# Optimization experiments

Hardware: AMD Instinct MI355X
Metric: run time of the kernel (lower is better)

Reference implementation:

```python
import jax, jax.numpy as jnp
import numpy as np

WINDOW = 16  # signature_window_size
D = 6        # input_path_dim


def _mlp(x, Ws, bs, final_act):
    for W, b in zip(Ws[:-1], bs[:-1]):
        x = jax.nn.softplus(W @ x + b)
    return final_act(Ws[-1] @ x + bs[-1])


def _windowed_logsig(xs):
    """Depth-2 log-signature of each window of the (piecewise-linear) path.
    Returns level-1 increments [n, D] and Levy areas [n, D, D] (antisymmetric)."""
    dx = xs[1:] - xs[:-1]                              # [T-1, D]
    n = dx.shape[0] // WINDOW
    dxw = dx[: n * WINDOW].reshape(n, WINDOW, D)
    lvl1 = dxw.sum(axis=1)                             # [n, D]
    cum = jnp.cumsum(dxw, axis=1) - dxw                # exclusive prefix sums
    cross = jnp.einsum('nwi,nwj->nij', cum, dxw)
    area = 0.5 * (cross - jnp.swapaxes(cross, 1, 2))   # [n, D, D]
    return lvl1, area


def setup_inputs() -> dict:
    key = jax.random.key(0)
    ks = jax.random.split(key, 9)
    S, H, OUT = 128, 128, 10
    B, T = 8, 513

    def lin(k, o, i):
        return jax.random.normal(k, (o, i), jnp.float32) / np.sqrt(i)

    return {
        'x': jax.random.normal(ks[0], (B, T, D), jnp.float32),
        'W_i0': lin(ks[1], H, D), 'b_i0': jnp.zeros((H,), jnp.float32),
        'W_i1': lin(ks[2], H, H), 'b_i1': jnp.zeros((H,), jnp.float32),
        'W_i2': lin(ks[3], S, H), 'b_i2': jnp.zeros((S,), jnp.float32),
        'W_v0': lin(ks[4], H, S), 'b_v0': jnp.zeros((H,), jnp.float32),
        'W_v1': lin(ks[5], H, H), 'b_v1': jnp.zeros((H,), jnp.float32),
        'W_v2': lin(ks[6], D * S, H), 'b_v2': jnp.zeros((D * S,), jnp.float32),
        'W_r': lin(ks[7], OUT, S), 'b_r': jnp.zeros((OUT,), jnp.float32),
    }


def reference(x, W_i0, b_i0, W_i1, b_i1, W_i2, b_i2,
              W_v0, b_v0, W_v1, b_v1, W_v2, b_v2, W_r, b_r):
    S = W_i2.shape[0]
    init_mlp = lambda z: _mlp(z, (W_i0, W_i1, W_i2), (b_i0, b_i1, b_i2), lambda u: u)
    # Vector fields V_i: R^S -> R^S, one per input channel (split_multi_vector_field)
    vf = lambda h: _mlp(h, (W_v0, W_v1, W_v2), (b_v0, b_v1, b_v2), jnp.tanh).reshape(D, S)
    mask = jnp.triu(jnp.ones((D, D), x.dtype), 1)  # Lyndon words i<j at depth 2

    def single(xs):  # xs: [T, D]
        lvl1, area = _windowed_logsig(xs)
        h0 = init_mlp(xs[0])

        def step(h, sig):
            l1, a = sig
            V = vf(h)                                  # [D, S]
            J = jax.jacfwd(vf)(h)                      # [D, S, S], J[j,b,a]=dV_j[b]/dh[a]
            M = jnp.einsum('jba,ia->ijb', J, V)        # (DV_j)(h) V_i(h)
            brack = M - jnp.swapaxes(M, 0, 1)          # Lie brackets [V_i, V_j](h)
            h_new = h + jnp.einsum('i,ib->b', l1, V) \
                      + jnp.einsum('ij,ijb->b', a * mask, brack)  # log-ODE step
            return h_new, h_new

        _, hist = jax.lax.scan(step, h0, (lvl1, area))
        hist = jnp.concatenate([h0[None], hist], axis=0)   # [n+1, S]
        return hist @ W_r.T + b_r                          # evolving readout

    return jax.vmap(single)(x)
```

## Files before the change

kernel.cpp:

```cpp
#include <hip/hip_runtime.h>
#include <math.h>

#define D    6
#define S    128
#define H    128
#define WIN  16
#define BB   8
#define TT   513
#define NW   32
#define OUTD 10

__device__ float g_lvl1[BB * NW * D];
__device__ float g_area[BB * NW * D * D];
__device__ float g_h0[BB * S];
__device__ float g_hist[BB * (NW + 1) * S];
__device__ float4 g_W2p[3 * 16 * 512];

__device__ __forceinline__ float sp(float x) {
    return (x > 20.f) ? x : log1pf(expf(x));
}
__device__ __forceinline__ float sigm(float x) {
    return 1.f / (1.f + expf(-x));
}
__device__ __forceinline__ float dot4(float4 a, float4 b, float acc) {
    return fmaf(a.x, b.x, fmaf(a.y, b.y, fmaf(a.z, b.z, fmaf(a.w, b.w, acc))));
}

#define O_W0   0
#define O_W1   16384
#define O_PS   32768
#define O_U    35840
#define O_T    36608
#define O_V    37376
#define O_H    38144
#define O_U1   38400
#define O_U2   38528
#define O_SG1  38656
#define O_SG2  38784
#define O_B0   38912
#define O_B1   39040
#define O_SIG  39168
#define SMTOT  39256

__global__ __launch_bounds__(512) void k_pack(const float* __restrict__ Wv2) {
    const float4* W24 = (const float4*)Wv2;
    int e = blockIdx.x * 512 + threadIdx.x;
    if (e < 3 * 16 * 512) {
        int ptr = e >> 13;
        int rem = e & 8191;
        int i   = rem >> 9;
        int tid = rem & 511;
        int r0 = tid >> 1, kh = tid & 1;
        int row = r0 + ptr * 256;
        g_W2p[e] = W24[row * 32 + kh * 16 + i];
    }
}

__global__ __launch_bounds__(256) void k_sig(
        const float* __restrict__ x,
        const float* __restrict__ Wi0, const float* __restrict__ bi0,
        const float* __restrict__ Wi1, const float* __restrict__ bi1,
        const float* __restrict__ Wi2, const float* __restrict__ bi2) {
    const int b = blockIdx.x;
    const int tid = threadIdx.x;
    __shared__ float dxs[NW][WIN][D];
    __shared__ float cums[NW][WIN][D];
    __shared__ float ua[H], ub[H];

    const float* xb = x + (size_t)b * TT * D;

    if (tid < NW * D) {
        int w = tid / D, i = tid % D;
        float run = 0.f;
        float prev = xb[(w * WIN) * D + i];
        for (int k = 0; k < WIN; ++k) {
            float cur = xb[(w * WIN + k + 1) * D + i];
            float d = cur - prev; prev = cur;
            dxs[w][k][i] = d;
            cums[w][k][i] = run;
            run += d;
        }
        g_lvl1[(b * NW + w) * D + i] = run;
    }
    __syncthreads();
    for (int e = tid; e < NW * D * D; e += blockDim.x) {
        int w = e / (D * D); int rem = e % (D * D);
        int i = rem / D, j = rem % D;
        float s = 0.f;
        for (int k = 0; k < WIN; ++k)
            s += cums[w][k][i] * dxs[w][k][j] - cums[w][k][j] * dxs[w][k][i];
        g_area[(b * NW + w) * (D * D) + rem] = 0.5f * s;
    }
    if (tid < H) {
        float z = bi0[tid];
        for (int k = 0; k < D; ++k) z += Wi0[tid * D + k] * xb[k];
        ua[tid] = sp(z);
    }
    __syncthreads();
    if (tid < H) {
        float z = bi1[tid];
        for (int k = 0; k < H; ++k) z += Wi1[tid * H + k] * ua[k];
        ub[tid] = sp(z);
    }
    __syncthreads();
    if (tid < H) {
        float z = bi2[tid];
        for (int k = 0; k < H; ++k) z += Wi2[tid * H + k] * ub[k];
        g_h0[b * S + tid] = z;
    }
}

__global__ __launch_bounds__(512, 2) void k_scan(
        const float* __restrict__ bv0, const float* __restrict__ bv1,
        const float* __restrict__ bv2,
        const float* __restrict__ Wv0, const float* __restrict__ Wv1) {
    __shared__ float sm[SMTOT];
    const int tid = threadIdx.x;
    const int b = blockIdx.x;
    const int r   = tid & 127;
    const int c4  = tid >> 7;
    const int key = r & 7;
    const int kh = tid & 1;
    const int r0 = tid >> 1, r1 = r0 + 256, r2 = r0 + 512;
    const int jA = tid >> 8, jB = 2 + jA, jC = 4 + jA;

    {
        float4* d = (float4*)(sm + O_W0);
        const float4* s0 = (const float4*)Wv0;
        const float4* s1 = (const float4*)Wv1;
        for (int i = tid; i < 4096; i += 512) { d[i] = s0[i]; d[4096 + i] = s1[i]; }
    }
    const float4* WAp = g_W2p + tid;
    const float4* WBp = g_W2p + 8192 + tid;
    const float4* WCp = g_W2p + 16384 + tid;
    if (tid < 128) {
        sm[O_B0 + tid] = bv0[tid]; sm[O_B1 + tid] = bv1[tid];
        float h0v = g_h0[b * 128 + tid];
        sm[O_H + tid] = h0v;
        g_hist[(b * (NW + 1)) * 128 + tid] = h0v;
    }
    if (tid >= 448) {
        int q = tid - 448;
        if (q < 42)
            sm[O_SIG + q] = (q < 6) ? g_lvl1[(b * NW) * 6 + q]
                                    : g_area[(b * NW) * 36 + q - 6];
    }
    __syncthreads();

    const float4* W04 = (const float4*)(sm + O_W0);
    const float4* W14 = (const float4*)(sm + O_W1);

    int p = 0;
    for (int t = 0; t < NW; ++t) {
        float rsig = 0.f;
        if (tid >= 448) {
            int q = tid - 448;
            if (q < 42 && t + 1 < NW)
                rsig = (q < 6) ? g_lvl1[(b * NW + t + 1) * 6 + q]
                               : g_area[(b * NW + t + 1) * 36 + q - 6];
        }
        const int sb = O_SIG + (t & 1) * 44;

        {
            float a = 0.f;
            const float4* H4 = (const float4*)(sm + O_H + p * 128);
            #pragma unroll
            for (int q = 0; q < 8; ++q) {
                int qq = c4 * 8 + (q ^ key);
                a = dot4(W04[r * 32 + qq], H4[qq], a);
            }
            sm[O_PS + (c4 * 6) * 128 + r] = a;
        }
        __syncthreads();
        if (tid < 128) {
            float z = sm[O_B0 + tid];
            #pragma unroll
            for (int c = 0; c < 4; ++c) z += sm[O_PS + (c * 6) * 128 + tid];
            sm[O_U1 + tid] = sp(z); sm[O_SG1 + tid] = sigm(z);
        }
        __syncthreads();
        {
            float a = 0.f;
            const float4* U14 = (const float4*)(sm + O_U1);
            #pragma unroll
            for (int q = 0; q < 8; ++q) {
                int qq = c4 * 8 + (q ^ key);
                a = dot4(W14[r * 32 + qq], U14[qq], a);
            }
            sm[O_PS + (c4 * 6) * 128 + r] = a;
        }
        __syncthreads();
        if (tid < 128) {
            float z = sm[O_B1 + tid];
            #pragma unroll
            for (int c = 0; c < 4; ++c) z += sm[O_PS + (c * 6) * 128 + tid];
            sm[O_U2 + tid] = sp(z); sm[O_SG2 + tid] = sigm(z);
        }
        __syncthreads();
        {
            float acc0 = 0.f, acc1 = 0.f, acc2 = 0.f;
            const float4* U24 = (const float4*)(sm + O_U2) + kh * 16;
            #pragma unroll 4
            for (int i = 0; i < 16; ++i) {
                float4 u = U24[i];
                acc0 = dot4(WAp[i * 512], u, acc0);
                acc1 = dot4(WBp[i * 512], u, acc1);
                acc2 = dot4(WCp[i * 512], u, acc2);
            }
            sm[O_PS + kh * 768 + r0] = acc0;
            sm[O_PS + kh * 768 + r1] = acc1;
            sm[O_PS + kh * 768 + r2] = acc2;
        }
        __syncthreads();
        {
            sm[O_V + tid] = tanhf(bv2[tid] + sm[O_PS + tid] + sm[O_PS + 768 + tid]);
            if (tid < 256) {
                int e = tid + 512;
                sm[O_V + e] = tanhf(bv2[e] + sm[O_PS + e] + sm[O_PS + 768 + e]);
            }
        }
        __syncthreads();
        {
            #pragma unroll
            for (int s = 0; s < 2; ++s) {
                int e = tid + s * 512;
                if (s == 0 || tid < 256) {
                    int jj = e >> 7, rr = e & 127;
                    float u = 0.f;
                    #pragma unroll
                    for (int i = 0; i < 6; ++i)
                        u = fmaf(sm[sb + 6 + i * 6 + jj], sm[O_V + i * 128 + rr], u);
                    sm[O_U + jj * 128 + rr] = u;
                }
            }
            if (tid < 128) {
                float xh = sm[O_H + p * 128 + tid];
                #pragma unroll
                for (int i = 0; i < 6; ++i)
                    xh = fmaf(sm[sb + i], sm[O_V + i * 128 + tid], xh);
                sm[O_H + (p ^ 1) * 128 + tid] = xh;
            }
        }
        __syncthreads();
        {
            float a0 = 0.f, a1 = 0.f, a2 = 0.f, a3 = 0.f, a4 = 0.f, a5 = 0.f;
            const float4* U4 = (const float4*)(sm + O_U);
            #pragma unroll
            for (int q = 0; q < 8; ++q) {
                int qq = c4 * 8 + (q ^ key);
                float4 w = W04[r * 32 + qq];
                a0 = dot4(w, U4[qq], a0);
                a1 = dot4(w, U4[32 + qq], a1);
                a2 = dot4(w, U4[64 + qq], a2);
                a3 = dot4(w, U4[96 + qq], a3);
                a4 = dot4(w, U4[128 + qq], a4);
                a5 = dot4(w, U4[160 + qq], a5);
            }
            sm[O_PS + (c4 * 6 + 0) * 128 + r] = a0;
            sm[O_PS + (c4 * 6 + 1) * 128 + r] = a1;
            sm[O_PS + (c4 * 6 + 2) * 128 + r] = a2;
            sm[O_PS + (c4 * 6 + 3) * 128 + r] = a3;
            sm[O_PS + (c4 * 6 + 4) * 128 + r] = a4;
            sm[O_PS + (c4 * 6 + 5) * 128 + r] = a5;
        }
        __syncthreads();
        {
            #pragma unroll
            for (int s = 0; s < 2; ++s) {
                int e = tid + s * 512;
                if (s == 0 || tid < 256) {
                    int jj = e >> 7, rr = e & 127;
                    float sv = sm[O_PS + jj * 128 + rr] + sm[O_PS + (6 + jj) * 128 + rr]
                             + sm[O_PS + (12 + jj) * 128 + rr] + sm[O_PS + (18 + jj) * 128 + rr];
                    sm[O_T + jj * 128 + rr] = sm[O_SG1 + rr] * sv;
                }
            }
        }
        __syncthreads();
        {
            float a0 = 0.f, a1 = 0.f, a2 = 0.f, a3 = 0.f, a4 = 0.f, a5 = 0.f;
            const float4* T4 = (const float4*)(sm + O_T);
            #pragma unroll
            for (int q = 0; q < 8; ++q) {
                int qq = c4 * 8 + (q ^ key);
                float4 w = W14[r * 32 + qq];
                a0 = dot4(w, T4[qq], a0);
                a1 = dot4(w, T4[32 + qq], a1);
                a2 = dot4(w, T4[64 + qq], a2);
                a3 = dot4(w, T4[96 + qq], a3);
                a4 = dot4(w, T4[128 + qq], a4);
                a5 = dot4(w, T4[160 + qq], a5);
            }
            sm[O_PS + (c4 * 6 + 0) * 128 + r] = a0;
            sm[O_PS + (c4 * 6 + 1) * 128 + r] = a1;
            sm[O_PS + (c4 * 6 + 2) * 128 + r] = a2;
            sm[O_PS + (c4 * 6 + 3) * 128 + r] = a3;
            sm[O_PS + (c4 * 6 + 4) * 128 + r] = a4;
            sm[O_PS + (c4 * 6 + 5) * 128 + r] = a5;
        }
        __syncthreads();
        {
            #pragma unroll
            for (int s = 0; s < 2; ++s) {
                int e = tid + s * 512;
                if (s == 0 || tid < 256) {
                    int jj = e >> 7, rr = e & 127;
                    float sv = sm[O_PS + jj * 128 + rr] + sm[O_PS + (6 + jj) * 128 + rr]
                             + sm[O_PS + (12 + jj) * 128 + rr] + sm[O_PS + (18 + jj) * 128 + rr];
                    sm[O_U + jj * 128 + rr] = sm[O_SG2 + rr] * sv;
                }
            }
        }
        __syncthreads();
        {
            float acc0 = 0.f, acc1 = 0.f, acc2 = 0.f;
            const float4* TA = (const float4*)(sm + O_U) + jA * 32 + kh * 16;
            const float4* TB = (const float4*)(sm + O_U) + jB * 32 + kh * 16;
            const float4* TC = (const float4*)(sm + O_U) + jC * 32 + kh * 16;
            #pragma unroll 4
            for (int i = 0; i < 16; ++i) {
                acc0 = dot4(WAp[i * 512], TA[i], acc0);
                acc1 = dot4(WBp[i * 512], TB[i], acc1);
                acc2 = dot4(WCp[i * 512], TC[i], acc2);
            }
            sm[O_PS + kh * 768 + r0] = acc0;
            sm[O_PS + kh * 768 + r1] = acc1;
            sm[O_PS + kh * 768 + r2] = acc2;
        }
        __syncthreads();
        {
            float v = sm[O_V + tid];
            sm[O_T + tid] = (1.f - v * v) * (sm[O_PS + tid] + sm[O_PS + 768 + tid]);
            if (tid < 256) {
                int e = tid + 512;
                float v2 = sm[O_V + e];
                sm[O_T + e] = (1.f - v2 * v2) * (sm[O_PS + e] + sm[O_PS + 768 + e]);
            }
        }
        __syncthreads();
        if (tid < 128) {
            float xh = sm[O_H + (p ^ 1) * 128 + tid];
            #pragma unroll
            for (int j = 0; j < 6; ++j) xh += sm[O_T + j * 128 + tid];
            sm[O_H + (p ^ 1) * 128 + tid] = xh;
            g_hist[(b * (NW + 1) + t + 1) * 128 + tid] = xh;
        }
        if (tid >= 448) {
            int q = tid - 448;
            if (q < 42 && t + 1 < NW)
                sm[O_SIG + ((t + 1) & 1) * 44 + q] = rsig;
        }
        p ^= 1;
        __syncthreads();
    }
}

__global__ __launch_bounds__(384) void k_read(const float* __restrict__ Wr,
                                              const float* __restrict__ br,
                                              float* __restrict__ out) {
    const int b = blockIdx.x, e = threadIdx.x;
    if (e < (NW + 1) * OUTD) {
        int t = e / OUTD, o = e % OUTD;
        float z = br[o];
        const float4* hrow = (const float4*)&g_hist[(b * (NW + 1) + t) * 128];
        const float4* wrow = (const float4*)&Wr[o * 128];
        float z0 = 0, z1 = 0, z2 = 0, z3 = 0;
        #pragma unroll 8
        for (int s4 = 0; s4 < 32; ++s4) {
            float4 hv = hrow[s4]; float4 wv = wrow[s4];
            z0 = fmaf(hv.x, wv.x, z0); z1 = fmaf(hv.y, wv.y, z1);
            z2 = fmaf(hv.z, wv.z, z2); z3 = fmaf(hv.w, wv.w, z3);
        }
        out[(b * (NW + 1) + t) * OUTD + o] = z + ((z0 + z1) + (z2 + z3));
    }
}

extern "C" void kernel_launch(void* const* d_in, const int* in_sizes, int n_in,
                              void* d_out, int out_size, void* d_ws, size_t ws_size,
                              hipStream_t stream) {
    const float* x   = (const float*)d_in[0];
    const float* Wi0 = (const float*)d_in[1];
    const float* bi0 = (const float*)d_in[2];
    const float* Wi1 = (const float*)d_in[3];
    const float* bi1 = (const float*)d_in[4];
    const float* Wi2 = (const float*)d_in[5];
    const float* bi2 = (const float*)d_in[6];
    const float* Wv0 = (const float*)d_in[7];
    const float* bv0 = (const float*)d_in[8];
    const float* Wv1 = (const float*)d_in[9];
    const float* bv1 = (const float*)d_in[10];
    const float* Wv2 = (const float*)d_in[11];
    const float* bv2 = (const float*)d_in[12];
    const float* Wr  = (const float*)d_in[13];
    const float* br  = (const float*)d_in[14];
    float* out = (float*)d_out;

    hipLaunchKernelGGL(k_pack, dim3(48), dim3(512), 0, stream, Wv2);
    hipLaunchKernelGGL(k_sig,  dim3(BB), dim3(256), 0, stream,
                       x, Wi0, bi0, Wi1, bi1, Wi2, bi2);
    hipLaunchKernelGGL(k_scan, dim3(BB), dim3(512), 0, stream,
                       bv0, bv1, bv2, Wv0, Wv1);
    hipLaunchKernelGGL(k_read, dim3(BB), dim3(384), 0, stream, Wr, br, out);
}
```

Measured before the change: 393.1 us.

## Replace shared-memory partial-sum reductions with wave shuffles and reassociate the area contraction

The scan kernel's thread mapping changes so the four partial dot products for each row sit in adjacent lanes and are combined with xor-shuffles. The bias, activation and tanh epilogues are folded into the matvec stages, which removes the partial-sum buffer and about half of the per-step block barriers. The area-weighted contraction is also moved to after the first-layer Jacobian matvec by linearity, and the h update is single-buffered. The cost is extra shuffle instructions, some idle lanes in the epilogues, and a different shared-memory access pattern for weight rows.

Result: slower. 438.2 us (+11.5%).

```diff
diff --git a/kernel.cpp b/kernel.cpp
--- a/kernel.cpp
+++ b/kernel.cpp
@@ -28,19 +28,19 @@
 
 #define O_W0   0
 #define O_W1   16384
-#define O_PS   32768
-#define O_U    35840
-#define O_T    36608
-#define O_V    37376
-#define O_H    38144
-#define O_U1   38400
-#define O_U2   38528
-#define O_SG1  38656
-#define O_SG2  38784
-#define O_B0   38912
-#define O_B1   39040
-#define O_SIG  39168
-#define SMTOT  39256
+#define O_V    32768
+#define O_T1   33536
+#define O_T2   34304
+#define O_H    35072
+#define O_U1   35200
+#define O_SG1  35328
+#define O_U2   35456
+#define O_SG2  35584
+#define O_B0   35712
+#define O_B1   35840
+#define O_B2   35968
+#define O_SIG  36736
+#define SMTOT  36824
 
 __global__ __launch_bounds__(512) void k_pack(const float* __restrict__ Wv2) {
     const float4* W24 = (const float4*)Wv2;
@@ -117,24 +117,26 @@
     __shared__ float sm[SMTOT];
     const int tid = threadIdx.x;
     const int b = blockIdx.x;
-    const int r   = tid & 127;
-    const int c4  = tid >> 7;
-    const int key = r & 7;
-    const int kh = tid & 1;
-    const int r0 = tid >> 1, r1 = r0 + 256, r2 = r0 + 512;
-    const int jA = tid >> 8, jB = 2 + jA, jC = 4 + jA;
+    const int r = tid >> 2, sub = tid & 3, key = r & 7;
+    const int kh = tid & 1, r0 = tid >> 1;
+    const int jA = r0 >> 7;
 
     {
         float4* d = (float4*)(sm + O_W0);
         const float4* s0 = (const float4*)Wv0;
         const float4* s1 = (const float4*)Wv1;
-        for (int i = tid; i < 4096; i += 512) { d[i] = s0[i]; d[4096 + i] = s1[i]; }
+        #pragma unroll
+        for (int i = 0; i < 8; ++i) d[tid + i * 512] = s0[tid + i * 512];
+        #pragma unroll
+        for (int i = 0; i < 8; ++i) d[4096 + tid + i * 512] = s1[tid + i * 512];
+        sm[O_B2 + tid] = bv2[tid];
+        if (tid < 256) sm[O_B2 + 512 + tid] = bv2[512 + tid];
+        if (tid < 128) { sm[O_B0 + tid] = bv0[tid]; sm[O_B1 + tid] = bv1[tid]; }
     }
     const float4* WAp = g_W2p + tid;
     const float4* WBp = g_W2p + 8192 + tid;
     const float4* WCp = g_W2p + 16384 + tid;
     if (tid < 128) {
-        sm[O_B0 + tid] = bv0[tid]; sm[O_B1 + tid] = bv1[tid];
         float h0v = g_h0[b * 128 + tid];
         sm[O_H + tid] = h0v;
         g_hist[(b * (NW + 1)) * 128 + tid] = h0v;
@@ -150,7 +152,6 @@
     const float4* W04 = (const float4*)(sm + O_W0);
     const float4* W14 = (const float4*)(sm + O_W1);
 
-    int p = 0;
     for (int t = 0; t < NW; ++t) {
         float rsig = 0.f;
         if (tid >= 448) {
@@ -163,20 +164,15 @@
 
         {
             float a = 0.f;
-            const float4* H4 = (const float4*)(sm + O_H + p * 128);
+            const float4* H4 = (const float4*)(sm + O_H);
             #pragma unroll
             for (int q = 0; q < 8; ++q) {
-                int qq = c4 * 8 + (q ^ key);
+                int qq = sub * 8 + (q ^ key);
                 a = dot4(W04[r * 32 + qq], H4[qq], a);
             }
-            sm[O_PS + (c4 * 6) * 128 + r] = a;
-        }
-        __syncthreads();
-        if (tid < 128) {
-            float z = sm[O_B0 + tid];
-            #pragma unroll
-            for (int c = 0; c < 4; ++c) z += sm[O_PS + (c * 6) * 128 + tid];
-            sm[O_U1 + tid] = sp(z); sm[O_SG1 + tid] = sigm(z);
+            a += __shfl_xor(a, 1); a += __shfl_xor(a, 2);
+            if (sub == 0)      sm[O_U1 + r]  = sp(sm[O_B0 + r] + a);
+            else if (sub == 1) sm[O_SG1 + r] = sigm(sm[O_B0 + r] + a);
         }
         __syncthreads();
         {
@@ -184,17 +180,12 @@
             const float4* U14 = (const float4*)(sm + O_U1);
             #pragma unroll
             for (int q = 0; q < 8; ++q) {
-                int qq = c4 * 8 + (q ^ key);
+                int qq = sub * 8 + (q ^ key);
                 a = dot4(W14[r * 32 + qq], U14[qq], a);
             }
-            sm[O_PS + (c4 * 6) * 128 + r] = a;
-        }
-        __syncthreads();
-        if (tid < 128) {
-            float z = sm[O_B1 + tid];
-            #pragma unroll
-            for (int c = 0; c < 4; ++c) z += sm[O_PS + (c * 6) * 128 + tid];
-            sm[O_U2 + tid] = sp(z); sm[O_SG2 + tid] = sigm(z);
+            a += __shfl_xor(a, 1); a += __shfl_xor(a, 2);
+            if (sub == 0)      sm[O_U2 + r]  = sp(sm[O_B1 + r] + a);
+            else if (sub == 1) sm[O_SG2 + r] = sigm(sm[O_B1 + r] + a);
         }
         __syncthreads();
         {
@@ -207,142 +198,124 @@
                 acc1 = dot4(WBp[i * 512], u, acc1);
                 acc2 = dot4(WCp[i * 512], u, acc2);
             }
-            sm[O_PS + kh * 768 + r0] = acc0;
-            sm[O_PS + kh * 768 + r1] = acc1;
-            sm[O_PS + kh * 768 + r2] = acc2;
-        }
-        __syncthreads();
-        {
-            sm[O_V + tid] = tanhf(bv2[tid] + sm[O_PS + tid] + sm[O_PS + 768 + tid]);
-            if (tid < 256) {
-                int e = tid + 512;
-                sm[O_V + e] = tanhf(bv2[e] + sm[O_PS + e] + sm[O_PS + 768 + e]);
-            }
-        }
-        __syncthreads();
-        {
-            #pragma unroll
-            for (int s = 0; s < 2; ++s) {
-                int e = tid + s * 512;
-                if (s == 0 || tid < 256) {
-                    int jj = e >> 7, rr = e & 127;
-                    float u = 0.f;
-                    #pragma unroll
-                    for (int i = 0; i < 6; ++i)
-                        u = fmaf(sm[sb + 6 + i * 6 + jj], sm[O_V + i * 128 + rr], u);
-                    sm[O_U + jj * 128 + rr] = u;
-                }
-            }
-            if (tid < 128) {
-                float xh = sm[O_H + p * 128 + tid];
-                #pragma unroll
-                for (int i = 0; i < 6; ++i)
-                    xh = fmaf(sm[sb + i], sm[O_V + i * 128 + tid], xh);
-                sm[O_H + (p ^ 1) * 128 + tid] = xh;
-            }
-        }
-        __syncthreads();
-        {
-            float a0 = 0.f, a1 = 0.f, a2 = 0.f, a3 = 0.f, a4 = 0.f, a5 = 0.f;
-            const float4* U4 = (const float4*)(sm + O_U);
+            acc0 += __shfl_xor(acc0, 1);
+            acc1 += __shfl_xor(acc1, 1);
+            acc2 += __shfl_xor(acc2, 1);
+            if (kh == 0) {
+                sm[O_V + r0]       = tanhf(sm[O_B2 + r0] + acc0);
+                sm[O_V + r0 + 256] = tanhf(sm[O_B2 + r0 + 256] + acc1);
+            } else {
+                sm[O_V + r0 + 512] = tanhf(sm[O_B2 + r0 + 512] + acc2);
+            }
+        }
+        __syncthreads();
+        {
+            float y0 = 0, y1 = 0, y2 = 0, y3 = 0, y4 = 0, y5 = 0;
+            const float4* V4 = (const float4*)(sm + O_V);
             #pragma unroll
             for (int q = 0; q < 8; ++q) {
-                int qq = c4 * 8 + (q ^ key);
+                int qq = sub * 8 + (q ^ key);
                 float4 w = W04[r * 32 + qq];
-                a0 = dot4(w, U4[qq], a0);
-                a1 = dot4(w, U4[32 + qq], a1);
-                a2 = dot4(w, U4[64 + qq], a2);
-                a3 = dot4(w, U4[96 + qq], a3);
-                a4 = dot4(w, U4[128 + qq], a4);
-                a5 = dot4(w, U4[160 + qq], a5);
-            }
-            sm[O_PS + (c4 * 6 + 0) * 128 + r] = a0;
-            sm[O_PS + (c4 * 6 + 1) * 128 + r] = a1;
-            sm[O_PS + (c4 * 6 + 2) * 128 + r] = a2;
-            sm[O_PS + (c4 * 6 + 3) * 128 + r] = a3;
-            sm[O_PS + (c4 * 6 + 4) * 128 + r] = a4;
-            sm[O_PS + (c4 * 6 + 5) * 128 + r] = a5;
-        }
-        __syncthreads();
-        {
-            #pragma unroll
-            for (int s = 0; s < 2; ++s) {
-                int e = tid + s * 512;
-                if (s == 0 || tid < 256) {
-                    int jj = e >> 7, rr = e & 127;
-                    float sv = sm[O_PS + jj * 128 + rr] + sm[O_PS + (6 + jj) * 128 + rr]
-                             + sm[O_PS + (12 + jj) * 128 + rr] + sm[O_PS + (18 + jj) * 128 + rr];
-                    sm[O_T + jj * 128 + rr] = sm[O_SG1 + rr] * sv;
-                }
-            }
-        }
-        __syncthreads();
-        {
-            float a0 = 0.f, a1 = 0.f, a2 = 0.f, a3 = 0.f, a4 = 0.f, a5 = 0.f;
-            const float4* T4 = (const float4*)(sm + O_T);
+                y0 = dot4(w, V4[qq], y0);
+                y1 = dot4(w, V4[32 + qq], y1);
+                y2 = dot4(w, V4[64 + qq], y2);
+                y3 = dot4(w, V4[96 + qq], y3);
+                y4 = dot4(w, V4[128 + qq], y4);
+                y5 = dot4(w, V4[160 + qq], y5);
+            }
+            y0 += __shfl_xor(y0, 1); y0 += __shfl_xor(y0, 2);
+            y1 += __shfl_xor(y1, 1); y1 += __shfl_xor(y1, 2);
+            y2 += __shfl_xor(y2, 1); y2 += __shfl_xor(y2, 2);
+            y3 += __shfl_xor(y3, 1); y3 += __shfl_xor(y3, 2);
+            y4 += __shfl_xor(y4, 1); y4 += __shfl_xor(y4, 2);
+            y5 += __shfl_xor(y5, 1); y5 += __shfl_xor(y5, 2);
+            if (sub < 3) {
+                const int j0 = 2 * sub, j1 = j0 + 1;
+                const float* A0 = sm + sb + 6;
+                float sg = sm[O_SG1 + r];
+                float t0 = fmaf(A0[j0], y0, 0.f);
+                t0 = fmaf(A0[6 + j0], y1, t0);
+                t0 = fmaf(A0[12 + j0], y2, t0);
+                t0 = fmaf(A0[18 + j0], y3, t0);
+                t0 = fmaf(A0[24 + j0], y4, t0);
+                t0 = fmaf(A0[30 + j0], y5, t0);
+                float t1 = fmaf(A0[j1], y0, 0.f);
+                t1 = fmaf(A0[6 + j1], y1, t1);
+                t1 = fmaf(A0[12 + j1], y2, t1);
+                t1 = fmaf(A0[18 + j1], y3, t1);
+                t1 = fmaf(A0[24 + j1], y4, t1);
+                t1 = fmaf(A0[30 + j1], y5, t1);
+                sm[O_T1 + j0 * 128 + r] = sg * t0;
+                sm[O_T1 + j1 * 128 + r] = sg * t1;
+            }
+        }
+        __syncthreads();
+        {
+            float z0 = 0, z1 = 0, z2 = 0, z3 = 0, z4 = 0, z5 = 0;
+            const float4* T4 = (const float4*)(sm + O_T1);
             #pragma unroll
             for (int q = 0; q < 8; ++q) {
-                int qq = c4 * 8 + (q ^ key);
+                int qq = sub * 8 + (q ^ key);
                 float4 w = W14[r * 32 + qq];
-                a0 = dot4(w, T4[qq], a0);
-                a1 = dot4(w, T4[32 + qq], a1);
-                a2 = dot4(w, T4[64 + qq], a2);
-                a3 = dot4(w, T4[96 + qq], a3);
-                a4 = dot4(w, T4[128 + qq], a4);
-                a5 = dot4(w, T4[160 + qq], a5);
-            }
-            sm[O_PS + (c4 * 6 + 0) * 128 + r] = a0;
-            sm[O_PS + (c4 * 6 + 1) * 128 + r] = a1;
-            sm[O_PS + (c4 * 6 + 2) * 128 + r] = a2;
-            sm[O_PS + (c4 * 6 + 3) * 128 + r] = a3;
-            sm[O_PS + (c4 * 6 + 4) * 128 + r] = a4;
-            sm[O_PS + (c4 * 6 + 5) * 128 + r] = a5;
-        }
-        __syncthreads();
-        {
-            #pragma unroll
-            for (int s = 0; s < 2; ++s) {
-                int e = tid + s * 512;
-                if (s == 0 || tid < 256) {
-                    int jj = e >> 7, rr = e & 127;
-                    float sv = sm[O_PS + jj * 128 + rr] + sm[O_PS + (6 + jj) * 128 + rr]
-                             + sm[O_PS + (12 + jj) * 128 + rr] + sm[O_PS + (18 + jj) * 128 + rr];
-                    sm[O_U + jj * 128 + rr] = sm[O_SG2 + rr] * sv;
-                }
+                z0 = dot4(w, T4[qq], z0);
+                z1 = dot4(w, T4[32 + qq], z1);
+                z2 = dot4(w, T4[64 + qq], z2);
+                z3 = dot4(w, T4[96 + qq], z3);
+                z4 = dot4(w, T4[128 + qq], z4);
+                z5 = dot4(w, T4[160 + qq], z5);
+            }
+            z0 += __shfl_xor(z0, 1); z0 += __shfl_xor(z0, 2);
+            z1 += __shfl_xor(z1, 1); z1 += __shfl_xor(z1, 2);
+            z2 += __shfl_xor(z2, 1); z2 += __shfl_xor(z2, 2);
+            z3 += __shfl_xor(z3, 1); z3 += __shfl_xor(z3, 2);
+            z4 += __shfl_xor(z4, 1); z4 += __shfl_xor(z4, 2);
+            z5 += __shfl_xor(z5, 1); z5 += __shfl_xor(z5, 2);
+            float sg = sm[O_SG2 + r];
+            if (sub == 0) {
+                sm[O_T2 + 0 * 128 + r] = sg * z0;
+                sm[O_T2 + 1 * 128 + r] = sg * z1;
+            } else if (sub == 1) {
+                sm[O_T2 + 2 * 128 + r] = sg * z2;
+                sm[O_T2 + 3 * 128 + r] = sg * z3;
+            } else if (sub == 2) {
+                sm[O_T2 + 4 * 128 + r] = sg * z4;
+                sm[O_T2 + 5 * 128 + r] = sg * z5;
             }
         }
         __syncthreads();
         {
             float acc0 = 0.f, acc1 = 0.f, acc2 = 0.f;
-            const float4* TA = (const float4*)(sm + O_U) + jA * 32 + kh * 16;
-            const float4* TB = (const float4*)(sm + O_U) + jB * 32 + kh * 16;
-            const float4* TC = (const float4*)(sm + O_U) + jC * 32 + kh * 16;
+            const float4* TA = (const float4*)(sm + O_T2) + jA * 32 + kh * 16;
+            const float4* TB = (const float4*)(sm + O_T2) + (2 + jA) * 32 + kh * 16;
+            const float4* TC = (const float4*)(sm + O_T2) + (4 + jA) * 32 + kh * 16;
             #pragma unroll 4
             for (int i = 0; i < 16; ++i) {
                 acc0 = dot4(WAp[i * 512], TA[i], acc0);
                 acc1 = dot4(WBp[i * 512], TB[i], acc1);
                 acc2 = dot4(WCp[i * 512], TC[i], acc2);
             }
-            sm[O_PS + kh * 768 + r0] = acc0;
-            sm[O_PS + kh * 768 + r1] = acc1;
-            sm[O_PS + kh * 768 + r2] = acc2;
-        }
-        __syncthreads();
-        {
-            float v = sm[O_V + tid];
-            sm[O_T + tid] = (1.f - v * v) * (sm[O_PS + tid] + sm[O_PS + 768 + tid]);
-            if (tid < 256) {
-                int e = tid + 512;
-                float v2 = sm[O_V + e];
-                sm[O_T + e] = (1.f - v2 * v2) * (sm[O_PS + e] + sm[O_PS + 768 + e]);
+            acc0 += __shfl_xor(acc0, 1);
+            acc1 += __shfl_xor(acc1, 1);
+            acc2 += __shfl_xor(acc2, 1);
+            if (kh == 0) {
+                float v0 = sm[O_V + r0];
+                float v1 = sm[O_V + r0 + 256];
+                sm[O_T1 + r0]       = (1.f - v0 * v0) * acc0;
+                sm[O_T1 + r0 + 256] = (1.f - v1 * v1) * acc1;
+            } else {
+                float v2 = sm[O_V + r0 + 512];
+                sm[O_T1 + r0 + 512] = (1.f - v2 * v2) * acc2;
             }
         }
         __syncthreads();
         if (tid < 128) {
-            float xh = sm[O_H + (p ^ 1) * 128 + tid];
-            #pragma unroll
-            for (int j = 0; j < 6; ++j) xh += sm[O_T + j * 128 + tid];
-            sm[O_H + (p ^ 1) * 128 + tid] = xh;
+            float xh = sm[O_H + tid];
+            #pragma unroll
+            for (int i = 0; i < 6; ++i)
+                xh = fmaf(sm[sb + i], sm[O_V + i * 128 + tid], xh);
+            #pragma unroll
+            for (int j = 0; j < 6; ++j) xh += sm[O_T1 + j * 128 + tid];
+            sm[O_H + tid] = xh;
             g_hist[(b * (NW + 1) + t + 1) * 128 + tid] = xh;
         }
         if (tid >= 448) {
@@ -350,7 +323,6 @@
             if (q < 42 && t + 1 < NW)
                 sm[O_SIG + ((t + 1) & 1) * 44 + q] = rsig;
         }
-        p ^= 1;
         __syncthreads();
     }
 }
```

## Apply area contraction after the W0 matvec and fuse the final update into the h step

Applied to the files above, without the earlier changes.

By linearity, the W_v0 product is now applied directly to the vector-field matrix V, and the antisymmetric area coefficients are contracted with the resulting partial sums afterwards. This removes the separate U-construction stage and its barrier. The tanh-derivative scaling and the h update are merged into a single 128-thread stage, which drops another barrier and the h ping-pong buffer. b_v2 is cached in shared memory. The merged tail stage runs on only 128 threads and does more serial work each, and the T stage now reads 24 partial sums per element.

After: 387.1 us, median of 2. Within noise of the previous version (-1.5%).

```diff
diff --git a/kernel.cpp b/kernel.cpp
--- a/kernel.cpp
+++ b/kernel.cpp
@@ -40,7 +40,8 @@
 #define O_B0   38912
 #define O_B1   39040
 #define O_SIG  39168
-#define SMTOT  39256
+#define O_B2   39256
+#define SMTOT  40024
 
 __global__ __launch_bounds__(512) void k_pack(const float* __restrict__ Wv2) {
     const float4* W24 = (const float4*)Wv2;
@@ -129,12 +130,14 @@
         const float4* s0 = (const float4*)Wv0;
         const float4* s1 = (const float4*)Wv1;
         for (int i = tid; i < 4096; i += 512) { d[i] = s0[i]; d[4096 + i] = s1[i]; }
+        sm[O_B2 + tid] = bv2[tid];
+        if (tid < 256) sm[O_B2 + 512 + tid] = bv2[512 + tid];
+        if (tid < 128) { sm[O_B0 + tid] = bv0[tid]; sm[O_B1 + tid] = bv1[tid]; }
     }
     const float4* WAp = g_W2p + tid;
     const float4* WBp = g_W2p + 8192 + tid;
     const float4* WCp = g_W2p + 16384 + tid;
     if (tid < 128) {
-        sm[O_B0 + tid] = bv0[tid]; sm[O_B1 + tid] = bv1[tid];
         float h0v = g_h0[b * 128 + tid];
         sm[O_H + tid] = h0v;
         g_hist[(b * (NW + 1)) * 128 + tid] = h0v;
@@ -150,7 +153,6 @@
     const float4* W04 = (const float4*)(sm + O_W0);
     const float4* W14 = (const float4*)(sm + O_W1);
 
-    int p = 0;
     for (int t = 0; t < NW; ++t) {
         float rsig = 0.f;
         if (tid >= 448) {
@@ -163,7 +165,7 @@
 
         {
             float a = 0.f;
-            const float4* H4 = (const float4*)(sm + O_H + p * 128);
+            const float4* H4 = (const float4*)(sm + O_H);
             #pragma unroll
             for (int q = 0; q < 8; ++q) {
                 int qq = c4 * 8 + (q ^ key);
@@ -213,48 +215,26 @@
         }
         __syncthreads();
         {
-            sm[O_V + tid] = tanhf(bv2[tid] + sm[O_PS + tid] + sm[O_PS + 768 + tid]);
+            sm[O_V + tid] = tanhf(sm[O_B2 + tid] + sm[O_PS + tid] + sm[O_PS + 768 + tid]);
             if (tid < 256) {
                 int e = tid + 512;
-                sm[O_V + e] = tanhf(bv2[e] + sm[O_PS + e] + sm[O_PS + 768 + e]);
-            }
-        }
-        __syncthreads();
-        {
-            #pragma unroll
-            for (int s = 0; s < 2; ++s) {
-                int e = tid + s * 512;
-                if (s == 0 || tid < 256) {
-                    int jj = e >> 7, rr = e & 127;
-                    float u = 0.f;
-                    #pragma unroll
-                    for (int i = 0; i < 6; ++i)
-                        u = fmaf(sm[sb + 6 + i * 6 + jj], sm[O_V + i * 128 + rr], u);
-                    sm[O_U + jj * 128 + rr] = u;
-                }
-            }
-            if (tid < 128) {
-                float xh = sm[O_H + p * 128 + tid];
-                #pragma unroll
-                for (int i = 0; i < 6; ++i)
-                    xh = fmaf(sm[sb + i], sm[O_V + i * 128 + tid], xh);
-                sm[O_H + (p ^ 1) * 128 + tid] = xh;
+                sm[O_V + e] = tanhf(sm[O_B2 + e] + sm[O_PS + e] + sm[O_PS + 768 + e]);
             }
         }
         __syncthreads();
         {
             float a0 = 0.f, a1 = 0.f, a2 = 0.f, a3 = 0.f, a4 = 0.f, a5 = 0.f;
-            const float4* U4 = (const float4*)(sm + O_U);
+            const float4* V4 = (const float4*)(sm + O_V);
             #pragma unroll
             for (int q = 0; q < 8; ++q) {
                 int qq = c4 * 8 + (q ^ key);
                 float4 w = W04[r * 32 + qq];
-                a0 = dot4(w, U4[qq], a0);
-                a1 = dot4(w, U4[32 + qq], a1);
-                a2 = dot4(w, U4[64 + qq], a2);
-                a3 = dot4(w, U4[96 + qq], a3);
-                a4 = dot4(w, U4[128 + qq], a4);
-                a5 = dot4(w, U4[160 + qq], a5);
+                a0 = dot4(w, V4[qq], a0);
+                a1 = dot4(w, V4[32 + qq], a1);
+                a2 = dot4(w, V4[64 + qq], a2);
+                a3 = dot4(w, V4[96 + qq], a3);
+                a4 = dot4(w, V4[128 + qq], a4);
+                a5 = dot4(w, V4[160 + qq], a5);
             }
             sm[O_PS + (c4 * 6 + 0) * 128 + r] = a0;
             sm[O_PS + (c4 * 6 + 1) * 128 + r] = a1;
@@ -270,8 +250,22 @@
                 int e = tid + s * 512;
                 if (s == 0 || tid < 256) {
                     int jj = e >> 7, rr = e & 127;
-                    float sv = sm[O_PS + jj * 128 + rr] + sm[O_PS + (6 + jj) * 128 + rr]
-                             + sm[O_PS + (12 + jj) * 128 + rr] + sm[O_PS + (18 + jj) * 128 + rr];
+                    float y0 = sm[O_PS + 0 * 128 + rr] + sm[O_PS + (6 + 0) * 128 + rr]
+                             + sm[O_PS + (12 + 0) * 128 + rr] + sm[O_PS + (18 + 0) * 128 + rr];
+                    float y1 = sm[O_PS + 1 * 128 + rr] + sm[O_PS + (6 + 1) * 128 + rr]
+                             + sm[O_PS + (12 + 1) * 128 + rr] + sm[O_PS + (18 + 1) * 128 + rr];
+                    float y2 = sm[O_PS + 2 * 128 + rr] + sm[O_PS + (6 + 2) * 128 + rr]
+                             + sm[O_PS + (12 + 2) * 128 + rr] + sm[O_PS + (18 + 2) * 128 + rr];
+                    float y3 = sm[O_PS + 3 * 128 + rr] + sm[O_PS + (6 + 3) * 128 + rr]
+                             + sm[O_PS + (12 + 3) * 128 + rr] + sm[O_PS + (18 + 3) * 128 + rr];
+                    float y4 = sm[O_PS + 4 * 128 + rr] + sm[O_PS + (6 + 4) * 128 + rr]
+                             + sm[O_PS + (12 + 4) * 128 + rr] + sm[O_PS + (18 + 4) * 128 + rr];
+                    float y5 = sm[O_PS + 5 * 128 + rr] + sm[O_PS + (6 + 5) * 128 + rr]
+                             + sm[O_PS + (12 + 5) * 128 + rr] + sm[O_PS + (18 + 5) * 128 + rr];
+                    const float* A0 = sm + sb + 6;
+                    float sv = A0[0 * 6 + jj] * y0 + A0[1 * 6 + jj] * y1
+                             + A0[2 * 6 + jj] * y2 + A0[3 * 6 + jj] * y3
+                             + A0[4 * 6 + jj] * y4 + A0[5 * 6 + jj] * y5;
                     sm[O_T + jj * 128 + rr] = sm[O_SG1 + rr] * sv;
                 }
             }
@@ -328,21 +322,17 @@
             sm[O_PS + kh * 768 + r2] = acc2;
         }
         __syncthreads();
-        {
-            float v = sm[O_V + tid];
-            sm[O_T + tid] = (1.f - v * v) * (sm[O_PS + tid] + sm[O_PS + 768 + tid]);
-            if (tid < 256) {
-                int e = tid + 512;
-                float v2 = sm[O_V + e];
-                sm[O_T + e] = (1.f - v2 * v2) * (sm[O_PS + e] + sm[O_PS + 768 + e]);
-            }
-        }
-        __syncthreads();
         if (tid < 128) {
-            float xh = sm[O_H + (p ^ 1) * 128 + tid];
-            #pragma unroll
-            for (int j = 0; j < 6; ++j) xh += sm[O_T + j * 128 + tid];
-            sm[O_H + (p ^ 1) * 128 + tid] = xh;
+            float xh = sm[O_H + tid];
+            #pragma unroll
+            for (int i = 0; i < 6; ++i)
+                xh = fmaf(sm[sb + i], sm[O_V + i * 128 + tid], xh);
+            #pragma unroll
+            for (int j = 0; j < 6; ++j) {
+                float v = sm[O_V + j * 128 + tid];
+                xh += (1.f - v * v) * (sm[O_PS + j * 128 + tid] + sm[O_PS + 768 + j * 128 + tid]);
+            }
+            sm[O_H + tid] = xh;
             g_hist[(b * (NW + 1) + t + 1) * 128 + tid] = xh;
         }
         if (tid >= 448) {
@@ -350,7 +340,6 @@
             if (q < 42 && t + 1 < NW)
                 sm[O_SIG + ((t + 1) & 1) * 44 + q] = rsig;
         }
-        p ^= 1;
         __syncthreads();
     }
 }
```
